# Optimization experiments

Hardware: AMD Instinct MI355X
Metric: run time of the kernel (lower is better)

The kernel has to match this reference:

```python
import jax, jax.numpy as jnp
import numpy as np

D = 128          # input_dim
H = 512          # hidden_dim = max(64, 4*D)
C = 10           # n_classes
T = 15           # n_trees
DEPTH = 3        # tree_depth
I = 2 ** DEPTH - 1   # n_internal = 7
L = 2 ** DEPTH       # n_leaves = 8
PPT = I * (D + 1) + L * C   # params_per_tree = 983
P = T * PPT                  # total_params = 14745
LN_EPS = 1e-5
B_TRAIN = 100000
B_TEST = 100000


def setup_inputs() -> dict:
    key = jax.random.key(0)
    ks = jax.random.split(key, 16)
    s = 0.02
    return {
        "X_train": jax.random.normal(ks[0], (B_TRAIN, D), jnp.float32),
        "X_test": jax.random.normal(ks[1], (B_TEST, D), jnp.float32),
        "enc_W1": jax.random.normal(ks[2], (H, D), jnp.float32) * s,
        "enc_b1": jnp.zeros((H,), jnp.float32),
        "ln1_g": jnp.ones((H,), jnp.float32),
        "ln1_b": jnp.zeros((H,), jnp.float32),
        "enc_W2": jax.random.normal(ks[3], (H, H), jnp.float32) * s,
        "enc_b2": jnp.zeros((H,), jnp.float32),
        "ln2_g": jnp.ones((H,), jnp.float32),
        "ln2_b": jnp.zeros((H,), jnp.float32),
        "head_W1": jax.random.normal(ks[4], (C, H, H), jnp.float32) * s,
        "head_b1": jnp.zeros((C, H), jnp.float32),
        "head_W2": jax.random.normal(ks[5], (C, P, H), jnp.float32) * s,
        "head_b2": jax.random.normal(ks[6], (C, P), jnp.float32) * s,
        "tree_weights": jnp.ones((T,), jnp.float32) / T,
    }


def _layernorm(x, g, b):
    m = x.mean(-1, keepdims=True)
    v = ((x - m) ** 2).mean(-1, keepdims=True)
    return (x - m) * jax.lax.rsqrt(v + LN_EPS) * g + b


def reference(X_train, X_test, enc_W1, enc_b1, ln1_g, ln1_b, enc_W2, enc_b2,
              ln2_g, ln2_b, head_W1, head_b1, head_W2, head_b2, tree_weights):
    # data encoder on the train-mean vector (dropout is identity in eval)
    mean = X_train.mean(0)                                  # [D]
    h = jax.nn.relu(_layernorm(enc_W1 @ mean + enc_b1, ln1_g, ln1_b))
    h = jax.nn.relu(_layernorm(enc_W2 @ h + enc_b2, ln2_g, ln2_b))   # [H]

    # all class heads at once: params [C, P]
    hh = jax.nn.relu(jnp.einsum('chd,d->ch', head_W1, h) + head_b1)
    params = jnp.einsum('cph,ch->cp', head_W2, hh) + head_b2

    # unpack per-tree params: [C, T, ...]
    p = params.reshape(C, T, PPT)
    split_w = p[..., :I * D].reshape(C, T, I, D)
    split_b = p[..., I * D:I * D + I]                       # [C, T, I]
    leaf_logits = p[..., I * D + I:].reshape(C, T, L, C)

    # soft routing (only the first DEPTH internal nodes are used, as in the source)
    routes = jax.nn.sigmoid(
        jnp.einsum('bd,ctid->ctbi', X_test, split_w) + split_b[:, :, None, :]
    )                                                       # [C, T, B, I]
    lp = jnp.ones(routes.shape[:3] + (1,), routes.dtype)    # [C, T, B, 1]
    for d in range(DEPTH):
        left = routes[..., d:d + 1]
        lp = jnp.concatenate([lp * left, lp * (1.0 - left)], axis=-1)
    # lp: [C, T, B, L]

    tree_out = jax.nn.softmax(leaf_logits, axis=-1)         # [C, T, L, C]
    probs = jnp.einsum('ctbl,ctlk->ctbk', lp[..., :L], tree_out)
    w = jax.nn.softmax(tree_weights)                        # [T]
    ens = jnp.einsum('t,ctbk->cbk', w, probs)               # per-head ensemble
    return ens.mean(0)                                      # [B, C]
```

## Files before the change

kernel.cpp:

```cpp
#include <hip/hip_runtime.h>

#define DD 128
#define NC 10
#define NT 15
#define NCT 150
#define NCOLS 450
#define BTRAIN 100000
#define BTEST 100000
#define GROWS 70050
#define NGRP 38

typedef __attribute__((ext_vector_type(8))) __bf16 bf16x8;
typedef __attribute__((ext_vector_type(4))) float f32x4;
typedef __attribute__((ext_vector_type(8))) unsigned short u16x8;

static __device__ __forceinline__ unsigned short f2bf(float f) {
  unsigned int u = __builtin_bit_cast(unsigned int, f);
  u = (u + 0x7FFFu + ((u >> 16) & 1u)) >> 16;
  return (unsigned short)u;
}

__global__ void __launch_bounds__(256) k_colsum(const float* __restrict__ X, float* __restrict__ partial) {
  int tid = threadIdx.x;
  int gid = blockIdx.x * 256 + tid;
  int stride = gridDim.x * 256;
  float sx = 0.f, sy = 0.f, sz = 0.f, sw = 0.f;
  const float4* Xv = (const float4*)X;
  for (int i = gid; i < BTRAIN * 32; i += stride) {
    float4 v = Xv[i];
    sx += v.x; sy += v.y; sz += v.z; sw += v.w;
  }
  __shared__ float red[256][4];
  red[tid][0] = sx; red[tid][1] = sy; red[tid][2] = sz; red[tid][3] = sw;
  __syncthreads();
  for (int off = 128; off >= 32; off >>= 1) {
    if (tid < off) {
      red[tid][0] += red[tid + off][0];
      red[tid][1] += red[tid + off][1];
      red[tid][2] += red[tid + off][2];
      red[tid][3] += red[tid + off][3];
    }
    __syncthreads();
  }
  if (tid < 32) {
#pragma unroll
    for (int i = 0; i < 4; ++i)
      partial[blockIdx.x * 128 + tid * 4 + i] = red[tid][i];
  }
}

__global__ void __launch_bounds__(256) k_z2(const float* __restrict__ partial,
                                            const float* __restrict__ W1, const float* __restrict__ b1,
                                            const float* __restrict__ g1, const float* __restrict__ bb1,
                                            const float* __restrict__ W2, const float* __restrict__ b2,
                                            float* __restrict__ z2g) {
  __shared__ float mS[128];
  __shared__ float redS[256];
  __shared__ float z1S[512];
  __shared__ float h1S[512];
  int tid = threadIdx.x;
  {
    int c = tid & 127, h = tid >> 7;
    float s = 0.0f;
    const float* pp = partial + (size_t)(h * 256) * 128 + c;
    for (int k = 0; k < 256; ++k) s += pp[k * 128];
    redS[tid] = s;
    __syncthreads();
    if (tid < 128) mS[tid] = (redS[tid] + redS[tid + 128]) * (1.0f / BTRAIN);
    __syncthreads();
  }
  for (int r = tid; r < 512; r += 256) {
    const float4* w = (const float4*)(W1 + (size_t)r * DD);
    float z = b1[r];
#pragma unroll
    for (int j = 0; j < 32; ++j) {
      float4 wv = w[j];
      z += wv.x * mS[4 * j] + wv.y * mS[4 * j + 1] + wv.z * mS[4 * j + 2] + wv.w * mS[4 * j + 3];
    }
    z1S[r] = z;
  }
  __syncthreads();
  {
    float a = z1S[tid], b = z1S[tid + 256];
    redS[tid] = a + b; __syncthreads();
    for (int off = 128; off > 0; off >>= 1) { if (tid < off) redS[tid] += redS[tid + off]; __syncthreads(); }
    float m = redS[0] * (1.0f / 512.0f); __syncthreads();
    float da = a - m, db = b - m;
    redS[tid] = da * da + db * db; __syncthreads();
    for (int off = 128; off > 0; off >>= 1) { if (tid < off) redS[tid] += redS[tid + off]; __syncthreads(); }
    float rs = rsqrtf(redS[0] * (1.0f / 512.0f) + 1e-5f); __syncthreads();
    h1S[tid] = fmaxf(da * rs * g1[tid] + bb1[tid], 0.0f);
    h1S[tid + 256] = fmaxf(db * rs * g1[tid + 256] + bb1[tid + 256], 0.0f);
  }
  __syncthreads();
  {
    int wv = tid >> 6, lane = tid & 63;
    int r = blockIdx.x * 4 + wv;
    const float4* wr = (const float4*)(W2 + (size_t)r * 512) + lane * 2;
    const float4* xv = (const float4*)h1S + lane * 2;
    float4 a0 = wr[0], a1 = wr[1], x0 = xv[0], x1 = xv[1];
    float s = a0.x * x0.x + a0.y * x0.y + a0.z * x0.z + a0.w * x0.w
            + a1.x * x1.x + a1.y * x1.y + a1.z * x1.z + a1.w * x1.w;
#pragma unroll
    for (int off = 32; off > 0; off >>= 1) s += __shfl_down(s, off);
    if (lane == 0) z2g[r] = s + b2[r];
  }
}

__global__ void __launch_bounds__(256) k_hh(const float* __restrict__ z2g,
                                            const float* __restrict__ g2, const float* __restrict__ bb2,
                                            const float* __restrict__ hW1, const float* __restrict__ hb1,
                                            float* __restrict__ hh) {
  __shared__ float redS[256];
  __shared__ float h2S[512];
  int tid = threadIdx.x;
  {
    float a = z2g[tid], b = z2g[tid + 256];
    redS[tid] = a + b; __syncthreads();
    for (int off = 128; off > 0; off >>= 1) { if (tid < off) redS[tid] += redS[tid + off]; __syncthreads(); }
    float m = redS[0] * (1.0f / 512.0f); __syncthreads();
    float da = a - m, db = b - m;
    redS[tid] = da * da + db * db; __syncthreads();
    for (int off = 128; off > 0; off >>= 1) { if (tid < off) redS[tid] += redS[tid + off]; __syncthreads(); }
    float rs = rsqrtf(redS[0] * (1.0f / 512.0f) + 1e-5f); __syncthreads();
    h2S[tid] = fmaxf(da * rs * g2[tid] + bb2[tid], 0.0f);
    h2S[tid + 256] = fmaxf(db * rs * g2[tid + 256] + bb2[tid + 256], 0.0f);
  }
  __syncthreads();
  int wv = tid >> 6, lane = tid & 63;
  const float4* xv = (const float4*)h2S + lane * 2;
  float4 x0 = xv[0], x1 = xv[1];
  float4 a[4][2];
  int r0 = blockIdx.x * 16 + wv * 4;
#pragma unroll
  for (int i = 0; i < 4; ++i) {
    const float4* wr = (const float4*)(hW1 + (size_t)(r0 + i) * 512) + lane * 2;
    a[i][0] = wr[0];
    a[i][1] = wr[1];
  }
#pragma unroll
  for (int i = 0; i < 4; ++i) {
    float s = a[i][0].x * x0.x + a[i][0].y * x0.y + a[i][0].z * x0.z + a[i][0].w * x0.w
            + a[i][1].x * x1.x + a[i][1].y * x1.y + a[i][1].z * x1.z + a[i][1].w * x1.w;
#pragma unroll
    for (int off = 32; off > 0; off >>= 1) s += __shfl_down(s, off);
    if (lane == 0) hh[r0 + i] = fmaxf(s + hb1[r0 + i], 0.0f);
  }
}

__global__ void __launch_bounds__(256) k_params(const float* __restrict__ W2, const float* __restrict__ hh,
                                                const float* __restrict__ b2, unsigned short* __restrict__ Wb,
                                                float* __restrict__ sb, float* __restrict__ leaf) {
  int wv = threadIdx.x >> 6, lane = threadIdx.x & 63;
  int base = (blockIdx.x * 4 + wv) * 8;
  if (base >= GROWS) return;
  float4 a[8][2];
  size_t rowoff[8];
  int ctArr[8], wArr[8], cArr[8];
#pragma unroll
  for (int i = 0; i < 8; ++i) {
    int R = base + i;
    if (R >= GROWS) R = GROWS - 1;
    int ctIdx = R / 467;
    int w = R - ctIdx * 467;
    int c = ctIdx / 15;
    int t = ctIdx - c * 15;
    int p;
    if (w < 384) p = t * 983 + w;
    else if (w < 387) p = t * 983 + 896 + (w - 384);
    else p = t * 983 + 903 + (w - 387);
    rowoff[i] = (size_t)c * 14745 + p;
    ctArr[i] = ctIdx; wArr[i] = w; cArr[i] = c;
    const float4* wr = (const float4*)(W2 + rowoff[i] * 512) + lane * 2;
    a[i][0] = wr[0];
    a[i][1] = wr[1];
  }
#pragma unroll
  for (int i = 0; i < 8; ++i) {
    const float4* xv = (const float4*)(hh + cArr[i] * 512) + lane * 2;
    float4 x0 = xv[0], x1 = xv[1];
    float s = a[i][0].x * x0.x + a[i][0].y * x0.y + a[i][0].z * x0.z + a[i][0].w * x0.w
            + a[i][1].x * x1.x + a[i][1].y * x1.y + a[i][1].z * x1.z + a[i][1].w * x1.w;
#pragma unroll
    for (int off = 32; off > 0; off >>= 1) s += __shfl_down(s, off);
    if (lane == 0) {
      s += b2[rowoff[i]];
      int w = wArr[i], ctIdx = ctArr[i];
      if (w < 384) {
        int ii = w >> 7, d = w & 127;
        Wb[(size_t)(ctIdx * 3 + ii) * DD + d] = f2bf(s);
      } else if (w < 387) {
        sb[ctIdx * 3 + (w - 384)] = s;
      } else {
        leaf[ctIdx * 80 + (w - 387)] = s;
      }
    }
  }
}

__global__ void k_tob(const float* __restrict__ leaf, const float* __restrict__ tw, unsigned short* __restrict__ TOB) {
  int g = blockIdx.x;
  int lane = threadIdx.x;
  int ct = g * 4 + (lane >> 4);
  int cls = lane & 15;
  float mx = tw[0];
  for (int i = 1; i < 15; ++i) mx = fmaxf(mx, tw[i]);
  float wsum = 0.0f;
  for (int i = 0; i < 15; ++i) wsum += __expf(tw[i] - mx);
  u16x8 o;
#pragma unroll
  for (int j = 0; j < 8; ++j) {
    float v = 0.0f;
    if (ct < NCT && cls < NC) {
      float wt = __expf(tw[ct % 15] - mx) / wsum;
      const float* lr = leaf + ct * 80 + j * 10;
      float m2 = lr[0];
#pragma unroll
      for (int k = 1; k < 10; ++k) m2 = fmaxf(m2, lr[k]);
      float es = 0.0f;
#pragma unroll
      for (int k = 0; k < 10; ++k) es += __expf(lr[k] - m2);
      v = __expf(lr[cls] - m2) / es * wt * (1.0f / (float)NC);
    }
    o[j] = f2bf(v);
  }
  *(u16x8*)&TOB[((size_t)g * 64 + lane) * 8] = o;
}

__global__ void __launch_bounds__(256) k_fused(const float* __restrict__ X, const unsigned short* __restrict__ Wb,
                                               const float* __restrict__ sb, const unsigned short* __restrict__ TOB,
                                               float* __restrict__ out) {
  __shared__ union {
    unsigned short Xs[64][152];
    _Float16 Rs[64][242];
  } sU;
  int tid = threadIdx.x;
  int b0 = blockIdx.x * 64;
  {
    int row = tid >> 2, seg = tid & 3;
    int gb = b0 + row;
    const float4* xr = (const float4*)(X + (size_t)gb * DD) + seg * 8;
#pragma unroll
    for (int j2 = 0; j2 < 4; ++j2) {
      bf16x8 u;
      if (gb < BTEST) {
        float4 va = xr[2 * j2], vb = xr[2 * j2 + 1];
        u[0] = (__bf16)va.x; u[1] = (__bf16)va.y; u[2] = (__bf16)va.z; u[3] = (__bf16)va.w;
        u[4] = (__bf16)vb.x; u[5] = (__bf16)vb.y; u[6] = (__bf16)vb.z; u[7] = (__bf16)vb.w;
      } else {
#pragma unroll
        for (int j = 0; j < 8; ++j) u[j] = (__bf16)0.0f;
      }
      *(u16x8*)&sU.Xs[row][seg * 32 + j2 * 8] = __builtin_bit_cast(u16x8, u);
    }
  }
  __syncthreads();
  int wv = tid >> 6, lane = tid & 63;
  int m = lane & 15, g = lane >> 4;
  bf16x8 A[4][4];
#pragma unroll
  for (int rt = 0; rt < 4; ++rt)
#pragma unroll
    for (int ks = 0; ks < 4; ++ks)
      A[rt][ks] = __builtin_bit_cast(bf16x8, *(const u16x8*)&sU.Xs[rt * 16 + m][ks * 32 + g * 8]);
  __syncthreads();
  f32x4 accA = 0.0f, accB = 0.0f;
  int pl = wv * 16 + m;
#pragma unroll
  for (int pass = 0; pass < 2; ++pass) {
    int passBase = pass ? 240 : 0;
    {
      int tstart, tcnt;
      if (pass == 0) { tstart = wv * 4; tcnt = (wv == 3) ? 3 : 4; }
      else { tstart = 15 + ((wv < 2) ? wv * 4 : (8 + (wv - 2) * 3)); tcnt = (wv < 2) ? 4 : 3; }
      int col = tstart * 16 + m;
      u16x8 Bv[4];
#pragma unroll
      for (int ks = 0; ks < 4; ++ks)
        Bv[ks] = *(const u16x8*)&Wb[(size_t)col * DD + ks * 32 + g * 8];
      float sbv = sb[col];
      for (int it = 0; it < tcnt; ++it) {
        int pc = (it + 1 < tcnt) ? (col + 16) : col;
        u16x8 Bn[4];
#pragma unroll
        for (int ks = 0; ks < 4; ++ks)
          Bn[ks] = *(const u16x8*)&Wb[(size_t)pc * DD + ks * 32 + g * 8];
        float sbn = sb[pc];
        f32x4 acc[4];
#pragma unroll
        for (int rt = 0; rt < 4; ++rt) acc[rt] = 0.0f;
#pragma unroll
        for (int ks = 0; ks < 4; ++ks) {
          bf16x8 Bf = __builtin_bit_cast(bf16x8, Bv[ks]);
#pragma unroll
          for (int rt = 0; rt < 4; ++rt)
            acc[rt] = __builtin_amdgcn_mfma_f32_16x16x32_bf16(A[rt][ks], Bf, acc[rt], 0, 0, 0);
        }
        int colLocal = col - passBase;
#pragma unroll
        for (int rt = 0; rt < 4; ++rt)
#pragma unroll
          for (int r = 0; r < 4; ++r) {
            float pre = acc[rt][r] + sbv;
            float e = __expf(-pre);
            float sg = __builtin_amdgcn_rcpf(1.0f + e);
            sU.Rs[rt * 16 + g * 4 + r][colLocal] = (_Float16)sg;
          }
#pragma unroll
        for (int ks = 0; ks < 4; ++ks) Bv[ks] = Bn[ks];
        sbv = sbn;
        col += 16;
      }
    }
    __syncthreads();
    {
      int gbase = pass ? 20 : 0;
      int gn = pass ? 18 : 20;
      int ctl = g;
      for (int gi = 0; gi < gn; ++gi) {
        int gAbs = gbase + gi;
        int ct = gAbs * 4 + ctl;
        int cb = 3 * ct - passBase;
        float l0 = (float)sU.Rs[pl][cb + 0];
        float l1 = (float)sU.Rs[pl][cb + 1];
        float l2 = (float)sU.Rs[pl][cb + 2];
        float n0 = 1.0f - l0, n1 = 1.0f - l1, n2 = 1.0f - l2;
        float p00 = l1 * l0, p01 = l1 * n0, p10 = n1 * l0, p11 = n1 * n0;
        bf16x8 av;
        av[0] = (__bf16)(l2 * p00); av[1] = (__bf16)(l2 * p01);
        av[2] = (__bf16)(l2 * p10); av[3] = (__bf16)(l2 * p11);
        av[4] = (__bf16)(n2 * p00); av[5] = (__bf16)(n2 * p01);
        av[6] = (__bf16)(n2 * p10); av[7] = (__bf16)(n2 * p11);
        u16x8 bv = *(const u16x8*)&TOB[((size_t)gAbs * 64 + lane) * 8];
        if (gi & 1)
          accB = __builtin_amdgcn_mfma_f32_16x16x32_bf16(av, __builtin_bit_cast(bf16x8, bv), accB, 0, 0, 0);
        else
          accA = __builtin_amdgcn_mfma_f32_16x16x32_bf16(av, __builtin_bit_cast(bf16x8, bv), accA, 0, 0, 0);
      }
    }
    __syncthreads();
  }
  f32x4 accT = accA + accB;
  int cls = lane & 15;
  if (cls < NC) {
#pragma unroll
    for (int r = 0; r < 4; ++r) {
      int b = b0 + wv * 16 + (lane >> 4) * 4 + r;
      if (b < BTEST) out[(size_t)b * 10 + cls] = accT[r];
    }
  }
}

extern "C" void kernel_launch(void* const* d_in, const int* in_sizes, int n_in,
                              void* d_out, int out_size, void* d_ws, size_t ws_size,
                              hipStream_t stream) {
  const float* Xtr = (const float*)d_in[0];
  const float* Xte = (const float*)d_in[1];
  const float* eW1 = (const float*)d_in[2];
  const float* eb1 = (const float*)d_in[3];
  const float* g1  = (const float*)d_in[4];
  const float* bb1 = (const float*)d_in[5];
  const float* eW2 = (const float*)d_in[6];
  const float* eb2 = (const float*)d_in[7];
  const float* g2  = (const float*)d_in[8];
  const float* bb2 = (const float*)d_in[9];
  const float* hW1 = (const float*)d_in[10];
  const float* hb1 = (const float*)d_in[11];
  const float* hW2 = (const float*)d_in[12];
  const float* hb2 = (const float*)d_in[13];
  const float* tw  = (const float*)d_in[14];

  char* ws = (char*)d_ws;
  const size_t OFF_PART = 0;
  const size_t OFF_Z2   = 262144;
  const size_t OFF_HH   = 264192;
  const size_t OFF_LEAF = 284672;
  const size_t OFF_SB   = 332672;
  const size_t OFF_WB   = 334528;
  const size_t OFF_TOB  = 453312;
  const size_t NEED     = 492224;
  if (ws_size < NEED) return;

  float* partial = (float*)(ws + OFF_PART);
  float* z2p = (float*)(ws + OFF_Z2);
  float* hhp = (float*)(ws + OFF_HH);
  float* leafp = (float*)(ws + OFF_LEAF);
  float* sbp = (float*)(ws + OFF_SB);
  unsigned short* Wb = (unsigned short*)(ws + OFF_WB);
  unsigned short* TOBp = (unsigned short*)(ws + OFF_TOB);

  k_colsum<<<512, 256, 0, stream>>>(Xtr, partial);
  k_z2<<<128, 256, 0, stream>>>(partial, eW1, eb1, g1, bb1, eW2, eb2, z2p);
  k_hh<<<320, 256, 0, stream>>>(z2p, g2, bb2, hW1, hb1, hhp);
  k_params<<<2190, 256, 0, stream>>>(hW2, hhp, hb2, Wb, sbp, leafp);
  k_tob<<<NGRP, 64, 0, stream>>>(leafp, tw, TOBp);
  k_fused<<<1563, 256, 0, stream>>>(Xte, Wb, sbp, TOBp, (float*)d_out);
}
```

Baseline: 130.2 us.

## Swap MFMA operands so routing sigmoids stay in registers, skipping the LDS round-trip

Split weights are repacked by k_params into a grouped, MFMA-fragment-ordered layout, 4 trees × 4 node slots per 16-row tile, with biases grouped the same way. The fused kernel now uses the weights as the A operand and the X tile as B. The first MFMA's output then lands in exactly the lane/register layout the leaf-probability MFMA needs. This removes the shared-memory staging of sigmoid results, the two-pass structure and its barriers. In exchange, one of the four node slots per tree is padding, so about a quarter of the routing MFMA work is wasted, and each wave now walks all 38 groups serially.

```diff
diff --git a/kernel.cpp b/kernel.cpp
--- a/kernel.cpp
+++ b/kernel.cpp
@@ -149,8 +149,8 @@
 }
 
 __global__ void __launch_bounds__(256) k_params(const float* __restrict__ W2, const float* __restrict__ hh,
-                                                const float* __restrict__ b2, unsigned short* __restrict__ Wb,
-                                                float* __restrict__ sb, float* __restrict__ leaf) {
+                                                const float* __restrict__ b2, unsigned short* __restrict__ WbF,
+                                                float* __restrict__ sbF, float* __restrict__ leaf) {
   int wv = threadIdx.x >> 6, lane = threadIdx.x & 63;
   int base = (blockIdx.x * 4 + wv) * 8;
   if (base >= GROWS) return;
@@ -186,11 +186,15 @@
     if (lane == 0) {
       s += b2[rowoff[i]];
       int w = wArr[i], ctIdx = ctArr[i];
+      int gi = ctIdx >> 2, gq = ctIdx & 3;
       if (w < 384) {
         int ii = w >> 7, d = w & 127;
-        Wb[(size_t)(ctIdx * 3 + ii) * DD + d] = f2bf(s);
+        int slot = gq * 4 + ii;
+        int ks = d >> 5, gp = (d >> 3) & 3, j = d & 7;
+        WbF[(((size_t)(gi * 4 + ks)) * 64 + gp * 16 + slot) * 8 + j] = f2bf(s);
       } else if (w < 387) {
-        sb[ctIdx * 3 + (w - 384)] = s;
+        int q = w - 384;
+        sbF[gi * 16 + gq * 4 + q] = s;
       } else {
         leaf[ctIdx * 80 + (w - 387)] = s;
       }
@@ -227,13 +231,10 @@
   *(u16x8*)&TOB[((size_t)g * 64 + lane) * 8] = o;
 }
 
-__global__ void __launch_bounds__(256) k_fused(const float* __restrict__ X, const unsigned short* __restrict__ Wb,
-                                               const float* __restrict__ sb, const unsigned short* __restrict__ TOB,
+__global__ void __launch_bounds__(256) k_fused(const float* __restrict__ X, const unsigned short* __restrict__ WbF,
+                                               const float* __restrict__ sbF, const unsigned short* __restrict__ TOB,
                                                float* __restrict__ out) {
-  __shared__ union {
-    unsigned short Xs[64][152];
-    _Float16 Rs[64][242];
-  } sU;
+  __shared__ unsigned short Xs[64][152];
   int tid = threadIdx.x;
   int b0 = blockIdx.x * 64;
   {
@@ -251,102 +252,61 @@
 #pragma unroll
         for (int j = 0; j < 8; ++j) u[j] = (__bf16)0.0f;
       }
-      *(u16x8*)&sU.Xs[row][seg * 32 + j2 * 8] = __builtin_bit_cast(u16x8, u);
+      *(u16x8*)&Xs[row][seg * 32 + j2 * 8] = __builtin_bit_cast(u16x8, u);
     }
   }
   __syncthreads();
   int wv = tid >> 6, lane = tid & 63;
   int m = lane & 15, g = lane >> 4;
-  bf16x8 A[4][4];
-#pragma unroll
-  for (int rt = 0; rt < 4; ++rt)
+  bf16x8 Bx[4];
+#pragma unroll
+  for (int ks = 0; ks < 4; ++ks)
+    Bx[ks] = __builtin_bit_cast(bf16x8, *(const u16x8*)&Xs[wv * 16 + m][ks * 32 + g * 8]);
+  f32x4 accA = 0.0f, accB = 0.0f;
+  u16x8 Wv[4];
+#pragma unroll
+  for (int ks = 0; ks < 4; ++ks)
+    Wv[ks] = *(const u16x8*)&WbF[((size_t)(0 * 4 + ks) * 64 + lane) * 8];
+  for (int gi = 0; gi < NGRP; ++gi) {
+    int gn = (gi + 1 < NGRP) ? gi + 1 : gi;
+    u16x8 Wn[4];
 #pragma unroll
     for (int ks = 0; ks < 4; ++ks)
-      A[rt][ks] = __builtin_bit_cast(bf16x8, *(const u16x8*)&sU.Xs[rt * 16 + m][ks * 32 + g * 8]);
-  __syncthreads();
-  f32x4 accA = 0.0f, accB = 0.0f;
-  int pl = wv * 16 + m;
-#pragma unroll
-  for (int pass = 0; pass < 2; ++pass) {
-    int passBase = pass ? 240 : 0;
-    {
-      int tstart, tcnt;
-      if (pass == 0) { tstart = wv * 4; tcnt = (wv == 3) ? 3 : 4; }
-      else { tstart = 15 + ((wv < 2) ? wv * 4 : (8 + (wv - 2) * 3)); tcnt = (wv < 2) ? 4 : 3; }
-      int col = tstart * 16 + m;
-      u16x8 Bv[4];
-#pragma unroll
-      for (int ks = 0; ks < 4; ++ks)
-        Bv[ks] = *(const u16x8*)&Wb[(size_t)col * DD + ks * 32 + g * 8];
-      float sbv = sb[col];
-      for (int it = 0; it < tcnt; ++it) {
-        int pc = (it + 1 < tcnt) ? (col + 16) : col;
-        u16x8 Bn[4];
-#pragma unroll
-        for (int ks = 0; ks < 4; ++ks)
-          Bn[ks] = *(const u16x8*)&Wb[(size_t)pc * DD + ks * 32 + g * 8];
-        float sbn = sb[pc];
-        f32x4 acc[4];
-#pragma unroll
-        for (int rt = 0; rt < 4; ++rt) acc[rt] = 0.0f;
-#pragma unroll
-        for (int ks = 0; ks < 4; ++ks) {
-          bf16x8 Bf = __builtin_bit_cast(bf16x8, Bv[ks]);
-#pragma unroll
-          for (int rt = 0; rt < 4; ++rt)
-            acc[rt] = __builtin_amdgcn_mfma_f32_16x16x32_bf16(A[rt][ks], Bf, acc[rt], 0, 0, 0);
-        }
-        int colLocal = col - passBase;
-#pragma unroll
-        for (int rt = 0; rt < 4; ++rt)
-#pragma unroll
-          for (int r = 0; r < 4; ++r) {
-            float pre = acc[rt][r] + sbv;
-            float e = __expf(-pre);
-            float sg = __builtin_amdgcn_rcpf(1.0f + e);
-            sU.Rs[rt * 16 + g * 4 + r][colLocal] = (_Float16)sg;
-          }
-#pragma unroll
-        for (int ks = 0; ks < 4; ++ks) Bv[ks] = Bn[ks];
-        sbv = sbn;
-        col += 16;
-      }
-    }
-    __syncthreads();
-    {
-      int gbase = pass ? 20 : 0;
-      int gn = pass ? 18 : 20;
-      int ctl = g;
-      for (int gi = 0; gi < gn; ++gi) {
-        int gAbs = gbase + gi;
-        int ct = gAbs * 4 + ctl;
-        int cb = 3 * ct - passBase;
-        float l0 = (float)sU.Rs[pl][cb + 0];
-        float l1 = (float)sU.Rs[pl][cb + 1];
-        float l2 = (float)sU.Rs[pl][cb + 2];
-        float n0 = 1.0f - l0, n1 = 1.0f - l1, n2 = 1.0f - l2;
-        float p00 = l1 * l0, p01 = l1 * n0, p10 = n1 * l0, p11 = n1 * n0;
-        bf16x8 av;
-        av[0] = (__bf16)(l2 * p00); av[1] = (__bf16)(l2 * p01);
-        av[2] = (__bf16)(l2 * p10); av[3] = (__bf16)(l2 * p11);
-        av[4] = (__bf16)(n2 * p00); av[5] = (__bf16)(n2 * p01);
-        av[6] = (__bf16)(n2 * p10); av[7] = (__bf16)(n2 * p11);
-        u16x8 bv = *(const u16x8*)&TOB[((size_t)gAbs * 64 + lane) * 8];
-        if (gi & 1)
-          accB = __builtin_amdgcn_mfma_f32_16x16x32_bf16(av, __builtin_bit_cast(bf16x8, bv), accB, 0, 0, 0);
-        else
-          accA = __builtin_amdgcn_mfma_f32_16x16x32_bf16(av, __builtin_bit_cast(bf16x8, bv), accA, 0, 0, 0);
-      }
-    }
-    __syncthreads();
+      Wn[ks] = *(const u16x8*)&WbF[((size_t)(gn * 4 + ks) * 64 + lane) * 8];
+    f32x4 acc = 0.0f;
+#pragma unroll
+    for (int ks = 0; ks < 4; ++ks)
+      acc = __builtin_amdgcn_mfma_f32_16x16x32_bf16(__builtin_bit_cast(bf16x8, Wv[ks]), Bx[ks], acc, 0, 0, 0);
+    float4 sbv = *(const float4*)&sbF[gi * 16 + g * 4];
+    float l0 = __builtin_amdgcn_rcpf(1.0f + __expf(-(acc[0] + sbv.x)));
+    float l1 = __builtin_amdgcn_rcpf(1.0f + __expf(-(acc[1] + sbv.y)));
+    float l2 = __builtin_amdgcn_rcpf(1.0f + __expf(-(acc[2] + sbv.z)));
+    float n0 = 1.0f - l0, n1 = 1.0f - l1, n2 = 1.0f - l2;
+    float p00 = l1 * l0, p01 = l1 * n0, p10 = n1 * l0, p11 = n1 * n0;
+    bool valid = (4 * gi + g) < NCT;
+    bf16x8 av;
+    av[0] = valid ? (__bf16)(l2 * p00) : (__bf16)0.0f;
+    av[1] = valid ? (__bf16)(l2 * p01) : (__bf16)0.0f;
+    av[2] = valid ? (__bf16)(l2 * p10) : (__bf16)0.0f;
+    av[3] = valid ? (__bf16)(l2 * p11) : (__bf16)0.0f;
+    av[4] = valid ? (__bf16)(n2 * p00) : (__bf16)0.0f;
+    av[5] = valid ? (__bf16)(n2 * p01) : (__bf16)0.0f;
+    av[6] = valid ? (__bf16)(n2 * p10) : (__bf16)0.0f;
+    av[7] = valid ? (__bf16)(n2 * p11) : (__bf16)0.0f;
+    u16x8 tb = *(const u16x8*)&TOB[((size_t)gi * 64 + lane) * 8];
+    if (gi & 1)
+      accB = __builtin_amdgcn_mfma_f32_16x16x32_bf16(av, __builtin_bit_cast(bf16x8, tb), accB, 0, 0, 0);
+    else
+      accA = __builtin_amdgcn_mfma_f32_16x16x32_bf16(av, __builtin_bit_cast(bf16x8, tb), accA, 0, 0, 0);
+#pragma unroll
+    for (int ks = 0; ks < 4; ++ks) Wv[ks] = Wn[ks];
   }
   f32x4 accT = accA + accB;
-  int cls = lane & 15;
-  if (cls < NC) {
+  if (m < NC) {
 #pragma unroll
     for (int r = 0; r < 4; ++r) {
-      int b = b0 + wv * 16 + (lane >> 4) * 4 + r;
-      if (b < BTEST) out[(size_t)b * 10 + cls] = accT[r];
+      int b = b0 + wv * 16 + g * 4 + r;
+      if (b < BTEST) out[(size_t)b * 10 + m] = accT[r];
     }
   }
 }
@@ -375,24 +335,24 @@
   const size_t OFF_Z2   = 262144;
   const size_t OFF_HH   = 264192;
   const size_t OFF_LEAF = 284672;
-  const size_t OFF_SB   = 332672;
-  const size_t OFF_WB   = 334528;
-  const size_t OFF_TOB  = 453312;
-  const size_t NEED     = 492224;
+  const size_t OFF_SBF  = 332672;
+  const size_t OFF_WBF  = 335104;
+  const size_t OFF_TOB  = 490752;
+  const size_t NEED     = 529664;
   if (ws_size < NEED) return;
 
   float* partial = (float*)(ws + OFF_PART);
   float* z2p = (float*)(ws + OFF_Z2);
   float* hhp = (float*)(ws + OFF_HH);
   float* leafp = (float*)(ws + OFF_LEAF);
-  float* sbp = (float*)(ws + OFF_SB);
-  unsigned short* Wb = (unsigned short*)(ws + OFF_WB);
+  float* sbFp = (float*)(ws + OFF_SBF);
+  unsigned short* WbFp = (unsigned short*)(ws + OFF_WBF);
   unsigned short* TOBp = (unsigned short*)(ws + OFF_TOB);
 
   k_colsum<<<512, 256, 0, stream>>>(Xtr, partial);
   k_z2<<<128, 256, 0, stream>>>(partial, eW1, eb1, g1, bb1, eW2, eb2, z2p);
   k_hh<<<320, 256, 0, stream>>>(z2p, g2, bb2, hW1, hb1, hhp);
-  k_params<<<2190, 256, 0, stream>>>(hW2, hhp, hb2, Wb, sbp, leafp);
+  k_params<<<2190, 256, 0, stream>>>(hW2, hhp, hb2, WbFp, sbFp, leafp);
   k_tob<<<NGRP, 64, 0, stream>>>(leafp, tw, TOBp);
-  k_fused<<<1563, 256, 0, stream>>>(Xte, Wb, sbp, TOBp, (float*)d_out);
-}
+  k_fused<<<1563, 256, 0, stream>>>(Xte, WbFp, sbFp, TOBp, (float*)d_out);
+}
```

Result: slower. 133.9 us (+2.9%).
